# Optimization experiments

Measured on AMD Instinct MI355X. Metric: run time of the kernel, lower is better.

## Reference

```python
import jax, jax.numpy as jnp
import numpy as np

NUM_USERS = 500000
NUM_ITEMS = 100000
D = 32
NUM_LAYERS = 3
AUDIO_SCALE = 1.0
META_SCALE = 0.5
NUM_ARTISTS = 50000
NUM_ALBUMS = 80000
E_BIP = 1000000


def l2norm(x, eps=1e-12):
    # matches torch F.normalize(p=2): x / max(||x||, eps)
    n = jnp.linalg.norm(x, axis=-1, keepdims=True)
    return x / jnp.maximum(n, eps)


def setup_inputs() -> dict:
    key = jax.random.key(0)
    ks = jax.random.split(key, 9)
    return {
        "user_emb_weight": jax.random.normal(ks[0], (NUM_USERS, D), dtype=jnp.float32),
        "item_audio_emb": jax.random.normal(ks[1], (NUM_ITEMS, D), dtype=jnp.float32),
        "artist_emb_weight": jax.random.normal(ks[2], (NUM_ARTISTS, D), dtype=jnp.float32),
        "album_emb_weight": jax.random.normal(ks[3], (NUM_ALBUMS, D), dtype=jnp.float32),
        "edge_weight": jax.random.uniform(ks[4], (E_BIP,), dtype=jnp.float32),
        "artist_ids": jax.random.randint(ks[5], (NUM_ITEMS,), 0, NUM_ARTISTS),
        "album_ids": jax.random.randint(ks[6], (NUM_ITEMS,), 0, NUM_ALBUMS),
        "edge_src": jax.random.randint(ks[7], (E_BIP,), 0, NUM_USERS),
        "edge_dst": jax.random.randint(ks[8], (E_BIP,), 0, NUM_ITEMS),
    }


def reference(user_emb_weight, item_audio_emb, artist_emb_weight, album_emb_weight,
              edge_weight, artist_ids, album_ids, edge_src, edge_dst):
    N = NUM_USERS + NUM_ITEMS
    # base embeddings
    user = l2norm(user_emb_weight)
    meta = artist_emb_weight[artist_ids] + album_emb_weight[album_ids]
    item = l2norm(item_audio_emb * AUDIO_SCALE + meta * META_SCALE)
    x = jnp.concatenate([user, item], axis=0)  # [N, D]

    # build homogeneous doubled edge list (items offset by NUM_USERS)
    src = jnp.concatenate([edge_src, edge_dst + NUM_USERS])
    dst = jnp.concatenate([edge_dst + NUM_USERS, edge_src])
    w = jnp.concatenate([edge_weight, edge_weight])[:, None]  # [2E, 1]

    acc = x
    for _ in range(NUM_LAYERS):
        # LGConv(normalize=False): out[dst] += w * x[src]
        x = jax.ops.segment_sum(w * x[src], dst, num_segments=N)
        acc = acc + x
    out = l2norm(acc / (NUM_LAYERS + 1))
    user_out = out[:NUM_USERS]
    item_out = out[NUM_USERS:]
    align_loss = jnp.float32(0.0)
    return user_out, item_out, align_loss
```

## Files before the change

### kernel.cpp

```cpp
#include <hip/hip_runtime.h>

constexpr int NUSERS = 500000;
constexpr int NITEMS = 100000;
constexpr int NNODES = NUSERS + NITEMS;
constexpr int EDGES  = 1000000;
constexpr int DIM    = 32;
constexpr long long XSZ = (long long)NNODES * DIM;

constexpr int RSZI = 1000;
constexpr int RI   = NITEMS / RSZI;
constexpr int RSZU = 2000;
constexpr int RU   = NUSERS / RSZU;
constexpr int CAPI = 10800;
constexpr int CAPU = 4600;
constexpr int SLICE = 4096;
constexpr int B1 = (EDGES + SLICE - 1) / SLICE;
constexpr int RBLK4 = (NNODES * 4 + 255) / 256;

using ushort8v = __attribute__((ext_vector_type(8))) unsigned short;
using float4v  = __attribute__((ext_vector_type(4))) float;

__device__ __forceinline__ float bf2f(unsigned short h) {
    return __uint_as_float((unsigned int)h << 16);
}
__device__ __forceinline__ unsigned short f2bf(float f) {
    unsigned int u = __float_as_uint(f);
    u = (u + 0x7FFFu + ((u >> 16) & 1u)) >> 16;
    return (unsigned short)u;
}

__device__ __forceinline__ unsigned int pack_rec(int src, float w) {
    unsigned int wq = (unsigned int)fminf(w * 4096.0f, 4095.0f);
    return ((unsigned int)src << 12) | wq;
}
__device__ __forceinline__ int   rec_src(unsigned int r) { return (int)(r >> 12); }
__device__ __forceinline__ float rec_w(unsigned int r) {
    return ((float)(r & 4095u) + 0.5f) * (1.0f / 4096.0f);
}

__global__ void hist_kernel(const int* __restrict__ esrc,
                            const int* __restrict__ edst,
                            int* __restrict__ histGI, int* __restrict__ histGU)
{
    __shared__ int histI[RI], histU[RU];
    int tid = threadIdx.x;
    for (int j = tid; j < RI; j += 256) histI[j] = 0;
    for (int j = tid; j < RU; j += 256) histU[j] = 0;
    __syncthreads();
    int base = blockIdx.x * SLICE;
    for (int k = 0; k < SLICE / 256; ++k) {
        int e = base + k * 256 + tid;
        if (e < EDGES) {
            atomicAdd(&histI[edst[e] / RSZI], 1);
            atomicAdd(&histU[esrc[e] / RSZU], 1);
        }
    }
    __syncthreads();
    for (int j = tid; j < RI; j += 256) histGI[j * B1 + blockIdx.x] = histI[j];
    for (int j = tid; j < RU; j += 256) histGU[j * B1 + blockIdx.x] = histU[j];
}

__global__ void base_kernel(int* __restrict__ histGI, int* __restrict__ histGU,
                            int* __restrict__ mGI, int* __restrict__ mGU)
{
    __shared__ int lds[256];
    bool item = blockIdx.x < RI;
    int r    = item ? blockIdx.x : blockIdx.x - RI;
    int* hG  = item ? histGI : histGU;
    int* mG  = item ? mGI : mGU;
    int cap  = item ? CAPI : CAPU;
    int tid  = threadIdx.x;
    int v = (tid < B1) ? hG[r * B1 + tid] : 0;
    lds[tid] = v;
    __syncthreads();
    for (int ofs = 1; ofs < 256; ofs <<= 1) {
        int add = (tid >= ofs) ? lds[tid - ofs] : 0;
        __syncthreads();
        lds[tid] += add;
        __syncthreads();
    }
    if (tid < B1) hG[r * B1 + tid] = r * cap + (lds[tid] - v);
    if (tid == 255) mG[r] = lds[255];
}

__global__ void scatter_kernel(
    const int* __restrict__ esrc, const int* __restrict__ edst,
    const float* __restrict__ ew,
    const int* __restrict__ baseGI, const int* __restrict__ baseGU,
    unsigned int* __restrict__ recBI, unsigned short* __restrict__ locBI,
    unsigned int* __restrict__ recBU, unsigned short* __restrict__ locBU)
{
    __shared__ int segI[RI], segU[RU], cntI[RI], cntU[RU];
    int tid = threadIdx.x;
    for (int j = tid; j < RI; j += 256) { segI[j] = baseGI[j * B1 + blockIdx.x]; cntI[j] = 0; }
    for (int j = tid; j < RU; j += 256) { segU[j] = baseGU[j * B1 + blockIdx.x]; cntU[j] = 0; }
    __syncthreads();
    int base = blockIdx.x * SLICE;
    for (int k = 0; k < SLICE / 256; ++k) {
        int e = base + k * 256 + tid;
        if (e < EDGES) {
            int u = esrc[e], d = edst[e];
            float w = ew[e];
            int rI = d / RSZI;
            int gI = segI[rI] + atomicAdd(&cntI[rI], 1);
            recBI[gI] = pack_rec(u, w);
            locBI[gI] = (unsigned short)(d - rI * RSZI);
            int rU = u / RSZU;
            int gU = segU[rU] + atomicAdd(&cntU[rU], 1);
            recBU[gU] = pack_rec(NUSERS + d, w);
            locBU[gU] = (unsigned short)(u - rU * RSZU);
        }
    }
}

__global__ void rbase_kernel(const int* __restrict__ mGI,
                             const int* __restrict__ mGU,
                             int* __restrict__ rbaseI, int* __restrict__ rbaseU,
                             int* __restrict__ offsI, int* __restrict__ offsU)
{
    int t = threadIdx.x;
    if (t == 0) {
        int s = 0;
        for (int j = 0; j < RI; ++j) { rbaseI[j] = s; s += mGI[j]; }
        rbaseI[RI] = s;
        offsI[NITEMS] = s;
    } else if (t == 64) {
        int s = 0;
        for (int j = 0; j < RU; ++j) { rbaseU[j] = s; s += mGU[j]; }
        rbaseU[RU] = s;
        offsU[NUSERS] = s;
    }
}

__global__ void finalize_csr_kernel(
    const int* __restrict__ mGI, const int* __restrict__ mGU,
    const int* __restrict__ rbaseI, const int* __restrict__ rbaseU,
    const unsigned int* __restrict__ recBI, const unsigned short* __restrict__ locBI,
    const unsigned int* __restrict__ recBU, const unsigned short* __restrict__ locBU,
    int* __restrict__ offsI, int* __restrict__ offsU,
    unsigned int* __restrict__ edI, unsigned int* __restrict__ edU)
{
    __shared__ int deg[RSZU];
    __shared__ int cur[RSZU];
    __shared__ int wsum[512];
    bool item = blockIdx.x < RI;
    int r   = item ? blockIdx.x : blockIdx.x - RI;
    int RSZ = item ? RSZI : RSZU;
    int cap = item ? CAPI : CAPU;
    int bstart = r * cap;
    int m   = item ? mGI[r] : mGU[r];
    int rb  = item ? rbaseI[r] : rbaseU[r];
    const unsigned int*   rec = item ? recBI : recBU;
    const unsigned short* loc = item ? locBI : locBU;
    int* offs = item ? offsI : offsU;
    unsigned int* ed = item ? edI : edU;
    int tid = threadIdx.x;

    for (int j = tid; j < RSZ; j += 512) { deg[j] = 0; cur[j] = 0; }
    __syncthreads();
    for (int k = tid; k < m; k += 512) atomicAdd(&deg[loc[bstart + k]], 1);
    __syncthreads();

    int b4 = tid * 4;
    int v0=0,v1=0,v2=0,v3=0;
    if (b4 + 0 < RSZ) v0 = deg[b4 + 0];
    if (b4 + 1 < RSZ) v1 = deg[b4 + 1];
    if (b4 + 2 < RSZ) v2 = deg[b4 + 2];
    if (b4 + 3 < RSZ) v3 = deg[b4 + 3];
    int lsum = v0 + v1 + v2 + v3;
    wsum[tid] = lsum; __syncthreads();
    for (int ofs = 1; ofs < 512; ofs <<= 1) {
        int add = (tid >= ofs) ? wsum[tid - ofs] : 0;
        __syncthreads();
        wsum[tid] += add;
        __syncthreads();
    }
    int s = wsum[tid] - lsum;
    if (b4 + 0 < RSZ) { deg[b4 + 0] = s; offs[r * RSZ + b4 + 0] = rb + s; s += v0; }
    if (b4 + 1 < RSZ) { deg[b4 + 1] = s; offs[r * RSZ + b4 + 1] = rb + s; s += v1; }
    if (b4 + 2 < RSZ) { deg[b4 + 2] = s; offs[r * RSZ + b4 + 2] = rb + s; s += v2; }
    if (b4 + 3 < RSZ) { deg[b4 + 3] = s; offs[r * RSZ + b4 + 3] = rb + s; s += v3; }
    __syncthreads();

    for (int k = tid; k < m; k += 512) {
        int l = loc[bstart + k];
        int pos = rb + deg[l] + atomicAdd(&cur[l], 1);
        ed[pos] = rec[bstart + k];
    }
}

__global__ void x0_kernel(
    const float* __restrict__ user_w,
    const float* __restrict__ audio,
    const float* __restrict__ artist_w,
    const float* __restrict__ album_w,
    const int*   __restrict__ artist_ids,
    const int*   __restrict__ album_ids,
    unsigned short* __restrict__ x)
{
    int t   = blockIdx.x * 256 + threadIdx.x;
    int row = t >> 2;
    if (row >= NNODES) return;
    int c = (t & 3) << 3;

    float v[8];
    if (row < NUSERS) {
        const float4v* p = (const float4v*)(user_w + (long long)row * DIM + c);
        float4v a = __builtin_nontemporal_load(p);
        float4v b = __builtin_nontemporal_load(p + 1);
        v[0]=a.x; v[1]=a.y; v[2]=a.z; v[3]=a.w;
        v[4]=b.x; v[5]=b.y; v[6]=b.z; v[7]=b.w;
    } else {
        int it = row - NUSERS;
        const float4v* pa = (const float4v*)(audio + (long long)it * DIM + c);
        int ar = artist_ids[it];
        int al = album_ids[it];
        const float* p1 = artist_w + (long long)ar * DIM + c;
        const float* p2 = album_w  + (long long)al * DIM + c;
        float4v a0 = __builtin_nontemporal_load(pa);
        float4v a1 = __builtin_nontemporal_load(pa + 1);
        float4 m0 = *(const float4*)p1,      m1 = *(const float4*)(p1 + 4);
        float4 n0 = *(const float4*)p2,      n1 = *(const float4*)(p2 + 4);
        v[0]=a0.x+0.5f*(m0.x+n0.x); v[1]=a0.y+0.5f*(m0.y+n0.y);
        v[2]=a0.z+0.5f*(m0.z+n0.z); v[3]=a0.w+0.5f*(m0.w+n0.w);
        v[4]=a1.x+0.5f*(m1.x+n1.x); v[5]=a1.y+0.5f*(m1.y+n1.y);
        v[6]=a1.z+0.5f*(m1.z+n1.z); v[7]=a1.w+0.5f*(m1.w+n1.w);
    }

    float ss = 0.f;
    #pragma unroll
    for (int j = 0; j < 8; ++j) ss += v[j] * v[j];
    ss += __shfl_xor(ss, 1);
    ss += __shfl_xor(ss, 2);
    float s = 1.0f / fmaxf(sqrtf(ss), 1e-12f);

    ushort8v hv;
    #pragma unroll
    for (int j = 0; j < 8; ++j) hv[j] = f2bf(v[j] * s);
    *(ushort8v*)(x + (long long)row * DIM + c) = hv;
}

__device__ __forceinline__ void gather_rows8(
    const unsigned int* __restrict__ ed, int b, int e,
    const unsigned short* __restrict__ xsrc, int c, float* __restrict__ sum)
{
    int k = b;
    for (; k + 3 < e; k += 4) {
        unsigned int r0 = ed[k], r1 = ed[k+1], r2 = ed[k+2], r3 = ed[k+3];
        float w0 = rec_w(r0), w1 = rec_w(r1), w2 = rec_w(r2), w3 = rec_w(r3);
        ushort8v xa = *(const ushort8v*)(xsrc + (long long)rec_src(r0) * DIM + c);
        ushort8v xb = *(const ushort8v*)(xsrc + (long long)rec_src(r1) * DIM + c);
        ushort8v xc = *(const ushort8v*)(xsrc + (long long)rec_src(r2) * DIM + c);
        ushort8v xd = *(const ushort8v*)(xsrc + (long long)rec_src(r3) * DIM + c);
        #pragma unroll
        for (int j = 0; j < 8; ++j)
            sum[j] += (w0 * bf2f(xa[j]) + w1 * bf2f(xb[j]))
                    + (w2 * bf2f(xc[j]) + w3 * bf2f(xd[j]));
    }
    for (; k + 1 < e; k += 2) {
        unsigned int r0 = ed[k], r1 = ed[k+1];
        float w0 = rec_w(r0), w1 = rec_w(r1);
        ushort8v xa = *(const ushort8v*)(xsrc + (long long)rec_src(r0) * DIM + c);
        ushort8v xb = *(const ushort8v*)(xsrc + (long long)rec_src(r1) * DIM + c);
        #pragma unroll
        for (int j = 0; j < 8; ++j)
            sum[j] += w0 * bf2f(xa[j]) + w1 * bf2f(xb[j]);
    }
    if (k < e) {
        unsigned int r0 = ed[k];
        float w0 = rec_w(r0);
        ushort8v xa = *(const ushort8v*)(xsrc + (long long)rec_src(r0) * DIM + c);
        #pragma unroll
        for (int j = 0; j < 8; ++j)
            sum[j] += w0 * bf2f(xa[j]);
    }
}

__global__ void layer_kernel(const int* __restrict__ offsU,
                             const int* __restrict__ offsI,
                             const unsigned int* __restrict__ edU,
                             const unsigned int* __restrict__ edI,
                             const unsigned short* __restrict__ xsrc,
                             unsigned short* __restrict__ xdst)
{
    int t = blockIdx.x * blockDim.x + threadIdx.x;
    int v = t >> 2;
    if (v >= NNODES) return;
    int c = (t & 3) << 3;

    const int* offs; const unsigned int* ed; int idx;
    if (v < NUSERS) { offs = offsU; ed = edU; idx = v; }
    else            { offs = offsI; ed = edI; idx = v - NUSERS; }
    int b = offs[idx], e = offs[idx + 1];

    float sum[8] = {0.f,0.f,0.f,0.f,0.f,0.f,0.f,0.f};
    gather_rows8(ed, b, e, xsrc, c, sum);

    ushort8v hv;
    #pragma unroll
    for (int j = 0; j < 8; ++j) hv[j] = f2bf(sum[j]);
    *(ushort8v*)(xdst + (long long)v * DIM + c) = hv;
}

__global__ void final_kernel(const int* __restrict__ offsU,
                             const int* __restrict__ offsI,
                             const unsigned int* __restrict__ edU,
                             const unsigned int* __restrict__ edI,
                             const unsigned short* __restrict__ x0,
                             const unsigned short* __restrict__ x1,
                             const unsigned short* __restrict__ x2,
                             float* __restrict__ out)
{
    int t = blockIdx.x * blockDim.x + threadIdx.x;
    if (t == 0) out[XSZ] = 0.0f;
    int v = t >> 2;
    if (v >= NNODES) return;
    int c = (t & 3) << 3;

    const int* offs; const unsigned int* ed; int idx;
    if (v < NUSERS) { offs = offsU; ed = edU; idx = v; }
    else            { offs = offsI; ed = edI; idx = v - NUSERS; }
    int b = offs[idx], e = offs[idx + 1];

    float sum[8] = {0.f,0.f,0.f,0.f,0.f,0.f,0.f,0.f};
    gather_rows8(ed, b, e, x2, c, sum);

    long long o = (long long)v * DIM + c;
    ushort8v a0 = __builtin_nontemporal_load((const ushort8v*)(x0 + o));
    ushort8v a1 = __builtin_nontemporal_load((const ushort8v*)(x1 + o));
    ushort8v a2 = *(const ushort8v*)(x2 + o);
    float acc[8];
    float ss = 0.f;
    #pragma unroll
    for (int j = 0; j < 8; ++j) {
        acc[j] = (bf2f(a0[j]) + bf2f(a1[j]) + bf2f(a2[j]) + sum[j]) * 0.25f;
        ss += acc[j] * acc[j];
    }
    ss += __shfl_xor(ss, 1);
    ss += __shfl_xor(ss, 2);
    float s = 1.0f / fmaxf(sqrtf(ss), 1e-12f);

    float4v o0 = { acc[0]*s, acc[1]*s, acc[2]*s, acc[3]*s };
    float4v o1 = { acc[4]*s, acc[5]*s, acc[6]*s, acc[7]*s };
    __builtin_nontemporal_store(o0, (float4v*)(out + o));
    __builtin_nontemporal_store(o1, (float4v*)(out + o + 4));
}

extern "C" void kernel_launch(void* const* d_in, const int* in_sizes, int n_in,
                              void* d_out, int out_size, void* d_ws, size_t ws_size,
                              hipStream_t stream)
{
    const float* user_w     = (const float*)d_in[0];
    const float* audio      = (const float*)d_in[1];
    const float* artist_w   = (const float*)d_in[2];
    const float* album_w    = (const float*)d_in[3];
    const float* ew         = (const float*)d_in[4];
    const int*   artist_ids = (const int*)d_in[5];
    const int*   album_ids  = (const int*)d_in[6];
    const int*   esrc       = (const int*)d_in[7];
    const int*   edst       = (const int*)d_in[8];
    float* out = (float*)d_out;

    unsigned short* x0 = (unsigned short*)d_ws;
    unsigned short* x1 = x0 + XSZ;
    unsigned short* x2 = x1 + XSZ;
    int* offsI = (int*)(x2 + XSZ);
    int* offsU = offsI + (NITEMS + 1);
    int* histGI = offsU + (NUSERS + 1);
    int* histGU = histGI + RI * B1;
    int* mGI    = histGU + RU * B1;
    int* mGU    = mGI + RI;
    int* rbaseI = mGU + RU;
    int* rbaseU = rbaseI + (RI + 1);
    unsigned int*   recBI = (unsigned int*)(rbaseU + (RU + 1));
    unsigned short* locBI = (unsigned short*)(recBI + (long long)RI * CAPI);
    unsigned int*   recBU = (unsigned int*)(locBI + (long long)RI * CAPI);
    unsigned short* locBU = (unsigned short*)(recBU + (long long)RU * CAPU);
    unsigned int*   edI   = (unsigned int*)(locBU + (long long)RU * CAPU);
    unsigned int*   edU   = edI + EDGES;

    const int THR = 256;

    hist_kernel<<<B1, THR, 0, stream>>>(esrc, edst, histGI, histGU);
    base_kernel<<<RI + RU, 256, 0, stream>>>(histGI, histGU, mGI, mGU);
    scatter_kernel<<<B1, THR, 0, stream>>>(
        esrc, edst, ew, histGI, histGU, recBI, locBI, recBU, locBU);
    rbase_kernel<<<1, 128, 0, stream>>>(mGI, mGU, rbaseI, rbaseU, offsI, offsU);
    finalize_csr_kernel<<<RI + RU, 512, 0, stream>>>(
        mGI, mGU, rbaseI, rbaseU,
        recBI, locBI, recBU, locBU, offsI, offsU, edI, edU);

    x0_kernel<<<RBLK4, THR, 0, stream>>>(
        user_w, audio, artist_w, album_w, artist_ids, album_ids, x0);

    layer_kernel<<<RBLK4, THR, 0, stream>>>(offsU, offsI, edU, edI, x0, x1);
    layer_kernel<<<RBLK4, THR, 0, stream>>>(offsU, offsI, edU, edI, x1, x2);
    final_kernel<<<RBLK4, THR, 0, stream>>>(offsU, offsI, edU, edI, x0, x1, x2, out);
}
```

Baseline: 233.6 us.

## Fold range-base prefix scan into CSR finalize and enlarge bucketing grid

Removes the single-threaded rbase_kernel, which scanned the per-range counts serially. Each finalize block now computes its own range base with a parallel block reduction over the preceding counts, and the total offset is written as the constant edge count. It also halves the edge slice per block and doubles the threads per block in the hist and scatter kernels, with the base scan widened to match. The cost is redundant summation of up to 250 counts in every finalize block and twice as many per-block histogram columns to scan.

```diff
diff --git a/kernel.cpp b/kernel.cpp
--- a/kernel.cpp
+++ b/kernel.cpp
@@ -13,7 +13,8 @@
 constexpr int RU   = NUSERS / RSZU;
 constexpr int CAPI = 10800;
 constexpr int CAPU = 4600;
-constexpr int SLICE = 4096;
+constexpr int BTHR  = 512;
+constexpr int SLICE = 2048;
 constexpr int B1 = (EDGES + SLICE - 1) / SLICE;
 constexpr int RBLK4 = (NNODES * 4 + 255) / 256;
 
@@ -44,26 +45,26 @@
 {
     __shared__ int histI[RI], histU[RU];
     int tid = threadIdx.x;
-    for (int j = tid; j < RI; j += 256) histI[j] = 0;
-    for (int j = tid; j < RU; j += 256) histU[j] = 0;
+    for (int j = tid; j < RI; j += BTHR) histI[j] = 0;
+    for (int j = tid; j < RU; j += BTHR) histU[j] = 0;
     __syncthreads();
     int base = blockIdx.x * SLICE;
-    for (int k = 0; k < SLICE / 256; ++k) {
-        int e = base + k * 256 + tid;
+    for (int k = 0; k < SLICE / BTHR; ++k) {
+        int e = base + k * BTHR + tid;
         if (e < EDGES) {
             atomicAdd(&histI[edst[e] / RSZI], 1);
             atomicAdd(&histU[esrc[e] / RSZU], 1);
         }
     }
     __syncthreads();
-    for (int j = tid; j < RI; j += 256) histGI[j * B1 + blockIdx.x] = histI[j];
-    for (int j = tid; j < RU; j += 256) histGU[j * B1 + blockIdx.x] = histU[j];
+    for (int j = tid; j < RI; j += BTHR) histGI[j * B1 + blockIdx.x] = histI[j];
+    for (int j = tid; j < RU; j += BTHR) histGU[j * B1 + blockIdx.x] = histU[j];
 }
 
 __global__ void base_kernel(int* __restrict__ histGI, int* __restrict__ histGU,
                             int* __restrict__ mGI, int* __restrict__ mGU)
 {
-    __shared__ int lds[256];
+    __shared__ int lds[512];
     bool item = blockIdx.x < RI;
     int r    = item ? blockIdx.x : blockIdx.x - RI;
     int* hG  = item ? histGI : histGU;
@@ -73,14 +74,14 @@
     int v = (tid < B1) ? hG[r * B1 + tid] : 0;
     lds[tid] = v;
     __syncthreads();
-    for (int ofs = 1; ofs < 256; ofs <<= 1) {
+    for (int ofs = 1; ofs < 512; ofs <<= 1) {
         int add = (tid >= ofs) ? lds[tid - ofs] : 0;
         __syncthreads();
         lds[tid] += add;
         __syncthreads();
     }
     if (tid < B1) hG[r * B1 + tid] = r * cap + (lds[tid] - v);
-    if (tid == 255) mG[r] = lds[255];
+    if (tid == 511) mG[r] = lds[511];
 }
 
 __global__ void scatter_kernel(
@@ -92,12 +93,12 @@
 {
     __shared__ int segI[RI], segU[RU], cntI[RI], cntU[RU];
     int tid = threadIdx.x;
-    for (int j = tid; j < RI; j += 256) { segI[j] = baseGI[j * B1 + blockIdx.x]; cntI[j] = 0; }
-    for (int j = tid; j < RU; j += 256) { segU[j] = baseGU[j * B1 + blockIdx.x]; cntU[j] = 0; }
+    for (int j = tid; j < RI; j += BTHR) { segI[j] = baseGI[j * B1 + blockIdx.x]; cntI[j] = 0; }
+    for (int j = tid; j < RU; j += BTHR) { segU[j] = baseGU[j * B1 + blockIdx.x]; cntU[j] = 0; }
     __syncthreads();
     int base = blockIdx.x * SLICE;
-    for (int k = 0; k < SLICE / 256; ++k) {
-        int e = base + k * 256 + tid;
+    for (int k = 0; k < SLICE / BTHR; ++k) {
+        int e = base + k * BTHR + tid;
         if (e < EDGES) {
             int u = esrc[e], d = edst[e];
             float w = ew[e];
@@ -113,28 +114,8 @@
     }
 }
 
-__global__ void rbase_kernel(const int* __restrict__ mGI,
-                             const int* __restrict__ mGU,
-                             int* __restrict__ rbaseI, int* __restrict__ rbaseU,
-                             int* __restrict__ offsI, int* __restrict__ offsU)
-{
-    int t = threadIdx.x;
-    if (t == 0) {
-        int s = 0;
-        for (int j = 0; j < RI; ++j) { rbaseI[j] = s; s += mGI[j]; }
-        rbaseI[RI] = s;
-        offsI[NITEMS] = s;
-    } else if (t == 64) {
-        int s = 0;
-        for (int j = 0; j < RU; ++j) { rbaseU[j] = s; s += mGU[j]; }
-        rbaseU[RU] = s;
-        offsU[NUSERS] = s;
-    }
-}
-
 __global__ void finalize_csr_kernel(
     const int* __restrict__ mGI, const int* __restrict__ mGU,
-    const int* __restrict__ rbaseI, const int* __restrict__ rbaseU,
     const unsigned int* __restrict__ recBI, const unsigned short* __restrict__ locBI,
     const unsigned int* __restrict__ recBU, const unsigned short* __restrict__ locBU,
     int* __restrict__ offsI, int* __restrict__ offsU,
@@ -148,13 +129,25 @@
     int RSZ = item ? RSZI : RSZU;
     int cap = item ? CAPI : CAPU;
     int bstart = r * cap;
-    int m   = item ? mGI[r] : mGU[r];
-    int rb  = item ? rbaseI[r] : rbaseU[r];
+    const int* mG = item ? mGI : mGU;
+    int m   = mG[r];
     const unsigned int*   rec = item ? recBI : recBU;
     const unsigned short* loc = item ? locBI : locBU;
     int* offs = item ? offsI : offsU;
     unsigned int* ed = item ? edI : edU;
     int tid = threadIdx.x;
+
+    int partial = 0;
+    for (int j = tid; j < r; j += 512) partial += mG[j];
+    wsum[tid] = partial; __syncthreads();
+    for (int ofs = 256; ofs > 0; ofs >>= 1) {
+        if (tid < ofs) wsum[tid] += wsum[tid + ofs];
+        __syncthreads();
+    }
+    int rb = wsum[0];
+    __syncthreads();
+
+    if (r == 0 && tid == 0) offs[item ? NITEMS : NUSERS] = EDGES;
 
     for (int j = tid; j < RSZ; j += 512) { deg[j] = 0; cur[j] = 0; }
     __syncthreads();
@@ -370,9 +363,7 @@
     int* histGU = histGI + RI * B1;
     int* mGI    = histGU + RU * B1;
     int* mGU    = mGI + RI;
-    int* rbaseI = mGU + RU;
-    int* rbaseU = rbaseI + (RI + 1);
-    unsigned int*   recBI = (unsigned int*)(rbaseU + (RU + 1));
+    unsigned int*   recBI = (unsigned int*)(mGU + RU);
     unsigned short* locBI = (unsigned short*)(recBI + (long long)RI * CAPI);
     unsigned int*   recBU = (unsigned int*)(locBI + (long long)RI * CAPI);
     unsigned short* locBU = (unsigned short*)(recBU + (long long)RU * CAPU);
@@ -381,14 +372,12 @@
 
     const int THR = 256;
 
-    hist_kernel<<<B1, THR, 0, stream>>>(esrc, edst, histGI, histGU);
-    base_kernel<<<RI + RU, 256, 0, stream>>>(histGI, histGU, mGI, mGU);
-    scatter_kernel<<<B1, THR, 0, stream>>>(
+    hist_kernel<<<B1, BTHR, 0, stream>>>(esrc, edst, histGI, histGU);
+    base_kernel<<<RI + RU, 512, 0, stream>>>(histGI, histGU, mGI, mGU);
+    scatter_kernel<<<B1, BTHR, 0, stream>>>(
         esrc, edst, ew, histGI, histGU, recBI, locBI, recBU, locBU);
-    rbase_kernel<<<1, 128, 0, stream>>>(mGI, mGU, rbaseI, rbaseU, offsI, offsU);
     finalize_csr_kernel<<<RI + RU, 512, 0, stream>>>(
-        mGI, mGU, rbaseI, rbaseU,
-        recBI, locBI, recBU, locBU, offsI, offsU, edI, edU);
+        mGI, mGU, recBI, locBI, recBU, locBU, offsI, offsU, edI, edU);
 
     x0_kernel<<<RBLK4, THR, 0, stream>>>(
         user_w, audio, artist_w, album_w, artist_ids, album_ids, x0);
```

After: 229.3 us, median of 2. Within noise of the previous version (-1.8%).
